# Kernel tuning notes

Hardware: AMD Instinct MI355X
Metric: run time of the kernel (lower is better)

The kernel has to match this reference:

```python
import jax, jax.numpy as jnp
import numpy as np

SIREN_OMEGA_0 = 30.0
EPS = 1e-4


def setup_inputs() -> dict:
    key = jax.random.key(0)
    ks = jax.random.split(key, 10)
    B, N, M, IN, OUT = 2, 16384, 1024, 256, 256
    x = jax.random.normal(ks[0], (B, N, IN), dtype=jnp.float32)
    query_coords = jax.random.normal(ks[1], (B, N, 3), dtype=jnp.float32)
    atomic_coords = jax.random.normal(ks[2], (B, M, 3), dtype=jnp.float32)
    # SIREN init (not is_first): bound = sqrt(6/in)/omega_0
    bound = (6.0 / IN) ** 0.5 / SIREN_OMEGA_0
    W = jax.random.uniform(ks[3], (OUT, IN), jnp.float32, -bound, bound)
    b = jax.random.uniform(ks[4], (OUT,), jnp.float32, -bound, bound)
    # freq_net: Linear(3,16) -> Softplus -> Linear(16,1), default torch init
    b1l = 1.0 / np.sqrt(3.0)
    fw1 = jax.random.uniform(ks[5], (16, 3), jnp.float32, -b1l, b1l)
    fb1 = jax.random.uniform(ks[6], (16,), jnp.float32, -b1l, b1l)
    b2l = 1.0 / np.sqrt(16.0)
    fw2 = jax.random.uniform(ks[7], (1, 16), jnp.float32, -b2l, b2l)
    fb2 = jax.random.uniform(ks[8], (1,), jnp.float32, -b2l, b2l)
    return {"x": x, "query_coords": query_coords, "atomic_coords": atomic_coords,
            "W": W, "b": b, "fw1": fw1, "fb1": fb1, "fw2": fw2, "fb2": fb2}


def reference(x, query_coords, atomic_coords, W, b, fw1, fb1, fw2, fb2):
    omega_base = SIREN_OMEGA_0
    # pre_activation = x @ W^T + b : [B, N, OUT]
    pre = jnp.einsum('bni,oi->bno', x, W) + b
    # freq_net(query_coords): Linear -> softplus -> Linear, clamp [0,5], nan->0
    h = jax.nn.softplus(jnp.einsum('bnd,hd->bnh', query_coords, fw1) + fb1)
    local_scale = jnp.einsum('bnh,oh->bno', h, fw2) + fb2  # [B, N, 1]
    local_scale = jnp.nan_to_num(jnp.clip(local_scale, 0.0, 5.0), nan=0.0)
    # pairwise distance [B, N, M] via broadcasted diff, then min over atoms
    diff = query_coords[:, :, None, :] - atomic_coords[:, None, :, :]  # [B,N,M,3]
    dist = jnp.sqrt(jnp.maximum(jnp.sum(diff * diff, axis=-1), EPS))
    min_dist = jnp.min(dist, axis=-1, keepdims=True)  # [B, N, 1]
    omega = omega_base * (1.0 + local_scale * jnp.exp(-min_dist))
    return jnp.sin(omega * pre)
```

## Files before the change

### kernel.cpp

```cpp
#include <hip/hip_runtime.h>
#include <hip/hip_bf16.h>

#define NPTS    32768
#define K_DIM   256
#define O_DIM   256
#define M_ATOMS 1024

typedef __attribute__((ext_vector_type(8))) short short8;
typedef __attribute__((ext_vector_type(4))) float f32x4;

__device__ __forceinline__ void split1(float v, short* h, short* l) {
  unsigned short hu = __bfloat16_as_ushort(__float2bfloat16(v));
  *h = (short)hu;
  float r = v - __uint_as_float((unsigned)hu << 16);
  *l = (short)__bfloat16_as_ushort(__float2bfloat16(r));
}

__device__ __forceinline__ void cvt8(const f32x4 f0, const f32x4 f1,
                                     short8* h, short8* l) {
#pragma unroll
  for (int j = 0; j < 4; ++j) {
    short hh, ll;
    split1(f0[j], &hh, &ll);
    (*h)[j] = hh; (*l)[j] = ll;
    split1(f1[j], &hh, &ll);
    (*h)[j + 4] = hh; (*l)[j + 4] = ll;
  }
}

__device__ __forceinline__ void async16(void* l, const void* g) {
  __builtin_amdgcn_global_load_lds(
      (const __attribute__((address_space(1))) void*)g,
      (__attribute__((address_space(3))) void*)l, 16, 0, 0);
}

__global__ __launch_bounds__(256) void wprep_kernel(const float* __restrict__ W,
                                                    unsigned short* __restrict__ whF,
                                                    unsigned short* __restrict__ wlF) {
  int t = blockIdx.x * 256 + threadIdx.x;
  int lane = t & 63;
  int ct = (t >> 6) & 15;
  int kc = t >> 10;
  int col = ct * 16 + (lane & 15);
  int k0 = kc * 32 + (lane >> 4) * 8;
  const float* src = W + (size_t)col * K_DIM + k0;
  f32x4 f0 = *(const f32x4*)(src);
  f32x4 f1 = *(const f32x4*)(src + 4);
  short8 h, l;
  cvt8(f0, f1, &h, &l);
  *(short8*)(whF + (size_t)t * 8) = h;
  *(short8*)(wlF + (size_t)t * 8) = l;
}

__global__ __launch_bounds__(512, 4) void fused_kernel(
    const float* __restrict__ x, const float* __restrict__ qc,
    const float* __restrict__ atoms,
    const unsigned short* __restrict__ whF, const unsigned short* __restrict__ wlF,
    const float* __restrict__ bias,
    const float* __restrict__ fw1, const float* __restrict__ fb1,
    const float* __restrict__ fw2, const float* __restrict__ fb2,
    float* __restrict__ out) {
  __shared__ char lds[65536];
  const int lane = threadIdx.x & 63;
  const int w = threadIdx.x >> 6;
  const int lrow = lane & 15;
  const int lk = lane >> 4;
  const int pb = (int)(blockIdx.x >> 2) * 256;
  const int cq = blockIdx.x & 3;
  const int pbase = pb + w * 32;

  {
    const char* whB = (const char*)whF;
    const char* wlB = (const char*)wlF;
    const int t = threadIdx.x;
    const int inner = (t & 255) * 16;
    const int kco = t >> 8;
#pragma unroll
    for (int p = 0; p < 4; ++p) {
      const int kc = p * 2 + kco;
      async16(lds + kc * 4096 + inner,
              whB + kc * 16384 + cq * 4096 + inner);
      async16(lds + 32768 + kc * 4096 + inner,
              wlB + kc * 16384 + cq * 4096 + inner);
    }
  }

  float bias_r[4];
#pragma unroll
  for (int ct = 0; ct < 4; ++ct) bias_r[ct] = bias[cq * 64 + ct * 16 + lrow];

  const float* xr0 = x + (size_t)(pbase + lrow) * K_DIM + lk * 8;
  const float* xr1 = xr0 + 16 * K_DIM;

  f32x4 c00 = *(const f32x4*)(xr0);
  f32x4 c01 = *(const f32x4*)(xr0 + 4);
  f32x4 c10 = *(const f32x4*)(xr1);
  f32x4 c11 = *(const f32x4*)(xr1 + 4);

  f32x4 acc[2][4];
#pragma unroll
  for (int t = 0; t < 2; ++t)
#pragma unroll
    for (int ct = 0; ct < 4; ++ct) acc[t][ct] = (f32x4){0.f, 0.f, 0.f, 0.f};

  __syncthreads();

#pragma unroll 1
  for (int kc = 0; kc < 8; ++kc) {
    f32x4 n00, n01, n10, n11;
    if (kc < 7) {
      const float* p0 = xr0 + (kc + 1) * 32;
      const float* p1 = xr1 + (kc + 1) * 32;
      n00 = *(const f32x4*)(p0); n01 = *(const f32x4*)(p0 + 4);
      n10 = *(const f32x4*)(p1); n11 = *(const f32x4*)(p1 + 4);
    }
    short8 ahi0, alo0, ahi1, alo1;
    cvt8(c00, c01, &ahi0, &alo0);
    cvt8(c10, c11, &ahi1, &alo1);
    const char* bp = lds + kc * 4096;
#pragma unroll
    for (int ct = 0; ct < 4; ++ct) {
      short8 bh = *(const short8*)(bp + ct * 1024 + lane * 16);
      short8 bl = *(const short8*)(bp + 32768 + ct * 1024 + lane * 16);
      acc[0][ct] = __builtin_amdgcn_mfma_f32_16x16x32_bf16(ahi0, bh, acc[0][ct], 0, 0, 0);
      acc[1][ct] = __builtin_amdgcn_mfma_f32_16x16x32_bf16(ahi1, bh, acc[1][ct], 0, 0, 0);
      acc[0][ct] = __builtin_amdgcn_mfma_f32_16x16x32_bf16(alo0, bh, acc[0][ct], 0, 0, 0);
      acc[1][ct] = __builtin_amdgcn_mfma_f32_16x16x32_bf16(alo1, bh, acc[1][ct], 0, 0, 0);
      acc[0][ct] = __builtin_amdgcn_mfma_f32_16x16x32_bf16(ahi0, bl, acc[0][ct], 0, 0, 0);
      acc[1][ct] = __builtin_amdgcn_mfma_f32_16x16x32_bf16(ahi1, bl, acc[1][ct], 0, 0, 0);
    }
    c00 = n00; c01 = n01; c10 = n10; c11 = n11;
  }

  __syncthreads();
  const int batch = pb >> 14;
  const float* A = atoms + (size_t)batch * M_ATOMS * 3;
  f32x4* at4 = (f32x4*)lds;
  {
    int i = threadIdx.x * 2;
    const float* ap = A + i * 3;
    float ax = ap[0], ay = ap[1], az = ap[2];
    at4[i] = (f32x4){ax, ay, az, ax * ax + ay * ay + az * az};
    ax = ap[3]; ay = ap[4]; az = ap[5];
    at4[i + 1] = (f32x4){ax, ay, az, ax * ax + ay * ay + az * az};
  }
  __syncthreads();

  const int pt = pbase + (lane & 31);
  const float qx = qc[(size_t)pt * 3 + 0];
  const float qy = qc[(size_t)pt * 3 + 1];
  const float qz = qc[(size_t)pt * 3 + 2];
  float m0 = 3.0e38f, m1 = 3.0e38f, m2 = 3.0e38f, m3 = 3.0e38f;
  const int i0 = (lane >> 5) * 512;
  for (int i = i0; i < i0 + 512; i += 4) {
    f32x4 v0 = at4[i + 0], v1 = at4[i + 1], v2 = at4[i + 2], v3 = at4[i + 3];
    float d;
    d = v0[0] * qx; d = __fmaf_rn(v0[1], qy, d); d = __fmaf_rn(v0[2], qz, d);
    m0 = fminf(m0, __fmaf_rn(d, -2.0f, v0[3]));
    d = v1[0] * qx; d = __fmaf_rn(v1[1], qy, d); d = __fmaf_rn(v1[2], qz, d);
    m1 = fminf(m1, __fmaf_rn(d, -2.0f, v1[3]));
    d = v2[0] * qx; d = __fmaf_rn(v2[1], qy, d); d = __fmaf_rn(v2[2], qz, d);
    m2 = fminf(m2, __fmaf_rn(d, -2.0f, v2[3]));
    d = v3[0] * qx; d = __fmaf_rn(v3[1], qy, d); d = __fmaf_rn(v3[2], qz, d);
    m3 = fminf(m3, __fmaf_rn(d, -2.0f, v3[3]));
  }
  float md = fminf(fminf(m0, m1), fminf(m2, m3));
  md = fminf(md, __shfl_xor(md, 32));
  md += qx * qx + qy * qy + qz * qz;
  float mind = sqrtf(fmaxf(md, 1.0e-4f));

  float facc = fb2[0];
#pragma unroll
  for (int j = 0; j < 16; ++j) {
    float z = fw1[j * 3 + 0] * qx + fw1[j * 3 + 1] * qy + fw1[j * 3 + 2] * qz + fb1[j];
    facc += fw2[j] * log1pf(__expf(z));
  }
  float ls = fminf(fmaxf(facc, 0.0f), 5.0f);
  float omega_l = 30.0f * (1.0f + ls * __expf(-mind));

  float om[2][4];
#pragma unroll
  for (int t = 0; t < 2; ++t)
#pragma unroll
    for (int j = 0; j < 4; ++j)
      om[t][j] = __shfl(omega_l, t * 16 + lk * 4 + j);

#pragma unroll
  for (int t = 0; t < 2; ++t) {
#pragma unroll
    for (int ct = 0; ct < 4; ++ct) {
#pragma unroll
      for (int j = 0; j < 4; ++j) {
        float pre = acc[t][ct][j] + bias_r[ct];
        out[(size_t)(pbase + t * 16 + lk * 4 + j) * O_DIM + cq * 64 + ct * 16 + lrow] =
            __sinf(om[t][j] * pre);
      }
    }
  }
}

extern "C" void kernel_launch(void* const* d_in, const int* in_sizes, int n_in,
                              void* d_out, int out_size, void* d_ws, size_t ws_size,
                              hipStream_t stream) {
  (void)in_sizes; (void)n_in; (void)out_size; (void)ws_size;
  const float* x     = (const float*)d_in[0];
  const float* qc    = (const float*)d_in[1];
  const float* atoms = (const float*)d_in[2];
  const float* W     = (const float*)d_in[3];
  const float* b     = (const float*)d_in[4];
  const float* fw1   = (const float*)d_in[5];
  const float* fb1   = (const float*)d_in[6];
  const float* fw2   = (const float*)d_in[7];
  const float* fb2   = (const float*)d_in[8];
  float* out = (float*)d_out;

  unsigned short* whF = (unsigned short*)d_ws;
  unsigned short* wlF = whF + 65536;

  wprep_kernel<<<32, 256, 0, stream>>>(W, whF, wlF);
  fused_kernel<<<512, 512, 0, stream>>>(x, qc, atoms, whF, wlF, b,
                                        fw1, fb1, fw2, fb2, out);
}
```

Measured before the change: 136.1 us.

## Restructure fused kernel into small 2-wave blocks with streamed per-k weight chunks

Each block now has 128 threads, and the grid grows to 2048 blocks, each covering 32 points by 128 output columns. Weight chunks are streamed into a small LDS buffer once per k-step instead of preloading the full 64KB. The distance minimum is split across both waves and combined through an LDS reduction. Block indices are swizzled, atom loads are vectorized, and softplus uses a stable max+log form. The aim is higher occupancy and less per-block LDS; the cost is more synchronisation per k-step and a redundant atom-distance scan per block.

```diff
diff --git a/kernel.cpp b/kernel.cpp
--- a/kernel.cpp
+++ b/kernel.cpp
@@ -52,7 +52,7 @@
   *(short8*)(wlF + (size_t)t * 8) = l;
 }
 
-__global__ __launch_bounds__(512, 4) void fused_kernel(
+__global__ __launch_bounds__(128, 4) void fused_kernel(
     const float* __restrict__ x, const float* __restrict__ qc,
     const float* __restrict__ atoms,
     const unsigned short* __restrict__ whF, const unsigned short* __restrict__ wlF,
@@ -60,99 +60,138 @@
     const float* __restrict__ fw1, const float* __restrict__ fb1,
     const float* __restrict__ fw2, const float* __restrict__ fb2,
     float* __restrict__ out) {
-  __shared__ char lds[65536];
+  __shared__ char lds[16640];
   const int lane = threadIdx.x & 63;
   const int w = threadIdx.x >> 6;
   const int lrow = lane & 15;
   const int lk = lane >> 4;
-  const int pb = (int)(blockIdx.x >> 2) * 256;
-  const int cq = blockIdx.x & 3;
-  const int pbase = pb + w * 32;
-
-  {
-    const char* whB = (const char*)whF;
-    const char* wlB = (const char*)wlF;
-    const int t = threadIdx.x;
-    const int inner = (t & 255) * 16;
-    const int kco = t >> 8;
-#pragma unroll
-    for (int p = 0; p < 4; ++p) {
-      const int kc = p * 2 + kco;
-      async16(lds + kc * 4096 + inner,
-              whB + kc * 16384 + cq * 4096 + inner);
-      async16(lds + 32768 + kc * 4096 + inner,
-              wlB + kc * 16384 + cq * 4096 + inner);
-    }
-  }
-
-  float bias_r[4];
-#pragma unroll
-  for (int ct = 0; ct < 4; ++ct) bias_r[ct] = bias[cq * 64 + ct * 16 + lrow];
+
+  const int p = blockIdx.x;
+  const int l = (p >> 3) + (p & 7) * 256;
+  const int u = l >> 1;
+  const int ch = l & 1;
+  const int pbase = u * 32;
+
+  const char* whB = (const char*)whF + ch * 8192;
+  const char* wlB = (const char*)wlF + ch * 8192;
+
+#pragma unroll
+  for (int r = 0; r < 4; ++r) {
+    async16(lds + r * 2048 + w * 1024,
+            whB + r * 2048 + w * 1024 + lane * 16);
+    async16(lds + 8192 + r * 2048 + w * 1024,
+            wlB + r * 2048 + w * 1024 + lane * 16);
+  }
 
   const float* xr0 = x + (size_t)(pbase + lrow) * K_DIM + lk * 8;
   const float* xr1 = xr0 + 16 * K_DIM;
 
-  f32x4 c00 = *(const f32x4*)(xr0);
-  f32x4 c01 = *(const f32x4*)(xr0 + 4);
-  f32x4 c10 = *(const f32x4*)(xr1);
-  f32x4 c11 = *(const f32x4*)(xr1 + 4);
-
-  f32x4 acc[2][4];
+  f32x4 c00 = *(const f32x4*)(xr0), c01 = *(const f32x4*)(xr0 + 4);
+  f32x4 c10 = *(const f32x4*)(xr1), c11 = *(const f32x4*)(xr1 + 4);
+
+  f32x4 acc[2][8];
 #pragma unroll
   for (int t = 0; t < 2; ++t)
 #pragma unroll
-    for (int ct = 0; ct < 4; ++ct) acc[t][ct] = (f32x4){0.f, 0.f, 0.f, 0.f};
-
-  __syncthreads();
+    for (int ct = 0; ct < 8; ++ct) acc[t][ct] = (f32x4){0.f, 0.f, 0.f, 0.f};
 
 #pragma unroll 1
   for (int kc = 0; kc < 8; ++kc) {
-    f32x4 n00, n01, n10, n11;
+    short8 ahi0, alo0, ahi1, alo1;
+    cvt8(c00, c01, &ahi0, &alo0);
+    cvt8(c10, c11, &ahi1, &alo1);
+    __syncthreads();
+
     if (kc < 7) {
       const float* p0 = xr0 + (kc + 1) * 32;
       const float* p1 = xr1 + (kc + 1) * 32;
-      n00 = *(const f32x4*)(p0); n01 = *(const f32x4*)(p0 + 4);
-      n10 = *(const f32x4*)(p1); n11 = *(const f32x4*)(p1 + 4);
-    }
-    short8 ahi0, alo0, ahi1, alo1;
-    cvt8(c00, c01, &ahi0, &alo0);
-    cvt8(c10, c11, &ahi1, &alo1);
-    const char* bp = lds + kc * 4096;
-#pragma unroll
-    for (int ct = 0; ct < 4; ++ct) {
-      short8 bh = *(const short8*)(bp + ct * 1024 + lane * 16);
-      short8 bl = *(const short8*)(bp + 32768 + ct * 1024 + lane * 16);
-      acc[0][ct] = __builtin_amdgcn_mfma_f32_16x16x32_bf16(ahi0, bh, acc[0][ct], 0, 0, 0);
-      acc[1][ct] = __builtin_amdgcn_mfma_f32_16x16x32_bf16(ahi1, bh, acc[1][ct], 0, 0, 0);
-      acc[0][ct] = __builtin_amdgcn_mfma_f32_16x16x32_bf16(alo0, bh, acc[0][ct], 0, 0, 0);
-      acc[1][ct] = __builtin_amdgcn_mfma_f32_16x16x32_bf16(alo1, bh, acc[1][ct], 0, 0, 0);
-      acc[0][ct] = __builtin_amdgcn_mfma_f32_16x16x32_bf16(ahi0, bl, acc[0][ct], 0, 0, 0);
-      acc[1][ct] = __builtin_amdgcn_mfma_f32_16x16x32_bf16(ahi1, bl, acc[1][ct], 0, 0, 0);
-    }
-    c00 = n00; c01 = n01; c10 = n10; c11 = n11;
-  }
-
-  __syncthreads();
-  const int batch = pb >> 14;
+      c00 = *(const f32x4*)(p0); c01 = *(const f32x4*)(p0 + 4);
+      c10 = *(const f32x4*)(p1); c11 = *(const f32x4*)(p1 + 4);
+    }
+
+#pragma unroll
+    for (int g = 0; g < 2; ++g) {
+      const char* bp = lds + g * 4096 + lane * 16;
+      short8 b0 = *(const short8*)(bp);
+      short8 b1 = *(const short8*)(bp + 1024);
+      short8 b2 = *(const short8*)(bp + 2048);
+      short8 b3 = *(const short8*)(bp + 3072);
+      const int c0 = g * 4;
+      acc[0][c0+0] = __builtin_amdgcn_mfma_f32_16x16x32_bf16(ahi0, b0, acc[0][c0+0], 0, 0, 0);
+      acc[0][c0+1] = __builtin_amdgcn_mfma_f32_16x16x32_bf16(ahi0, b1, acc[0][c0+1], 0, 0, 0);
+      acc[0][c0+2] = __builtin_amdgcn_mfma_f32_16x16x32_bf16(ahi0, b2, acc[0][c0+2], 0, 0, 0);
+      acc[0][c0+3] = __builtin_amdgcn_mfma_f32_16x16x32_bf16(ahi0, b3, acc[0][c0+3], 0, 0, 0);
+      acc[1][c0+0] = __builtin_amdgcn_mfma_f32_16x16x32_bf16(ahi1, b0, acc[1][c0+0], 0, 0, 0);
+      acc[1][c0+1] = __builtin_amdgcn_mfma_f32_16x16x32_bf16(ahi1, b1, acc[1][c0+1], 0, 0, 0);
+      acc[1][c0+2] = __builtin_amdgcn_mfma_f32_16x16x32_bf16(ahi1, b2, acc[1][c0+2], 0, 0, 0);
+      acc[1][c0+3] = __builtin_amdgcn_mfma_f32_16x16x32_bf16(ahi1, b3, acc[1][c0+3], 0, 0, 0);
+      acc[0][c0+0] = __builtin_amdgcn_mfma_f32_16x16x32_bf16(alo0, b0, acc[0][c0+0], 0, 0, 0);
+      acc[0][c0+1] = __builtin_amdgcn_mfma_f32_16x16x32_bf16(alo0, b1, acc[0][c0+1], 0, 0, 0);
+      acc[0][c0+2] = __builtin_amdgcn_mfma_f32_16x16x32_bf16(alo0, b2, acc[0][c0+2], 0, 0, 0);
+      acc[0][c0+3] = __builtin_amdgcn_mfma_f32_16x16x32_bf16(alo0, b3, acc[0][c0+3], 0, 0, 0);
+      acc[1][c0+0] = __builtin_amdgcn_mfma_f32_16x16x32_bf16(alo1, b0, acc[1][c0+0], 0, 0, 0);
+      acc[1][c0+1] = __builtin_amdgcn_mfma_f32_16x16x32_bf16(alo1, b1, acc[1][c0+1], 0, 0, 0);
+      acc[1][c0+2] = __builtin_amdgcn_mfma_f32_16x16x32_bf16(alo1, b2, acc[1][c0+2], 0, 0, 0);
+      acc[1][c0+3] = __builtin_amdgcn_mfma_f32_16x16x32_bf16(alo1, b3, acc[1][c0+3], 0, 0, 0);
+    }
+#pragma unroll
+    for (int g = 0; g < 2; ++g) {
+      const char* bp = lds + 8192 + g * 4096 + lane * 16;
+      short8 b0 = *(const short8*)(bp);
+      short8 b1 = *(const short8*)(bp + 1024);
+      short8 b2 = *(const short8*)(bp + 2048);
+      short8 b3 = *(const short8*)(bp + 3072);
+      const int c0 = g * 4;
+      acc[0][c0+0] = __builtin_amdgcn_mfma_f32_16x16x32_bf16(ahi0, b0, acc[0][c0+0], 0, 0, 0);
+      acc[0][c0+1] = __builtin_amdgcn_mfma_f32_16x16x32_bf16(ahi0, b1, acc[0][c0+1], 0, 0, 0);
+      acc[0][c0+2] = __builtin_amdgcn_mfma_f32_16x16x32_bf16(ahi0, b2, acc[0][c0+2], 0, 0, 0);
+      acc[0][c0+3] = __builtin_amdgcn_mfma_f32_16x16x32_bf16(ahi0, b3, acc[0][c0+3], 0, 0, 0);
+      acc[1][c0+0] = __builtin_amdgcn_mfma_f32_16x16x32_bf16(ahi1, b0, acc[1][c0+0], 0, 0, 0);
+      acc[1][c0+1] = __builtin_amdgcn_mfma_f32_16x16x32_bf16(ahi1, b1, acc[1][c0+1], 0, 0, 0);
+      acc[1][c0+2] = __builtin_amdgcn_mfma_f32_16x16x32_bf16(ahi1, b2, acc[1][c0+2], 0, 0, 0);
+      acc[1][c0+3] = __builtin_amdgcn_mfma_f32_16x16x32_bf16(ahi1, b3, acc[1][c0+3], 0, 0, 0);
+    }
+    __syncthreads();
+    if (kc < 7) {
+      const char* gh = whB + (kc + 1) * 16384;
+      const char* gl = wlB + (kc + 1) * 16384;
+#pragma unroll
+      for (int r = 0; r < 4; ++r) {
+        async16(lds + r * 2048 + w * 1024,
+                gh + r * 2048 + w * 1024 + lane * 16);
+        async16(lds + 8192 + r * 2048 + w * 1024,
+                gl + r * 2048 + w * 1024 + lane * 16);
+      }
+    }
+  }
+
+  const int batch = pbase >> 14;
   const float* A = atoms + (size_t)batch * M_ATOMS * 3;
   f32x4* at4 = (f32x4*)lds;
   {
-    int i = threadIdx.x * 2;
-    const float* ap = A + i * 3;
-    float ax = ap[0], ay = ap[1], az = ap[2];
-    at4[i] = (f32x4){ax, ay, az, ax * ax + ay * ay + az * az};
-    ax = ap[3]; ay = ap[4]; az = ap[5];
-    at4[i + 1] = (f32x4){ax, ay, az, ax * ax + ay * ay + az * az};
+    const int t = threadIdx.x;
+    const f32x4* ap = (const f32x4*)(A + t * 24);
+    f32x4 a0 = ap[0], a1 = ap[1], a2 = ap[2], a3 = ap[3], a4 = ap[4], a5 = ap[5];
+    f32x4* d = at4 + t * 8;
+    d[0] = (f32x4){a0[0], a0[1], a0[2], a0[0]*a0[0] + a0[1]*a0[1] + a0[2]*a0[2]};
+    d[1] = (f32x4){a0[3], a1[0], a1[1], a0[3]*a0[3] + a1[0]*a1[0] + a1[1]*a1[1]};
+    d[2] = (f32x4){a1[2], a1[3], a2[0], a1[2]*a1[2] + a1[3]*a1[3] + a2[0]*a2[0]};
+    d[3] = (f32x4){a2[1], a2[2], a2[3], a2[1]*a2[1] + a2[2]*a2[2] + a2[3]*a2[3]};
+    d[4] = (f32x4){a3[0], a3[1], a3[2], a3[0]*a3[0] + a3[1]*a3[1] + a3[2]*a3[2]};
+    d[5] = (f32x4){a3[3], a4[0], a4[1], a3[3]*a3[3] + a4[0]*a4[0] + a4[1]*a4[1]};
+    d[6] = (f32x4){a4[2], a4[3], a5[0], a4[2]*a4[2] + a4[3]*a4[3] + a5[0]*a5[0]};
+    d[7] = (f32x4){a5[1], a5[2], a5[3], a5[1]*a5[1] + a5[2]*a5[2] + a5[3]*a5[3]};
   }
   __syncthreads();
 
-  const int pt = pbase + (lane & 31);
+  const int pp = lane & 31;
+  const int pt = pbase + pp;
   const float qx = qc[(size_t)pt * 3 + 0];
   const float qy = qc[(size_t)pt * 3 + 1];
   const float qz = qc[(size_t)pt * 3 + 2];
   float m0 = 3.0e38f, m1 = 3.0e38f, m2 = 3.0e38f, m3 = 3.0e38f;
-  const int i0 = (lane >> 5) * 512;
-  for (int i = i0; i < i0 + 512; i += 4) {
+  const int i0 = w * 512 + (lane >> 5) * 256;
+  for (int i = i0; i < i0 + 256; i += 4) {
     f32x4 v0 = at4[i + 0], v1 = at4[i + 1], v2 = at4[i + 2], v3 = at4[i + 3];
     float d;
     d = v0[0] * qx; d = __fmaf_rn(v0[1], qy, d); d = __fmaf_rn(v0[2], qz, d);
@@ -166,6 +205,10 @@
   }
   float md = fminf(fminf(m0, m1), fminf(m2, m3));
   md = fminf(md, __shfl_xor(md, 32));
+  float* red = (float*)(lds + 16384);
+  if (lane < 32) red[w * 32 + lane] = md;
+  __syncthreads();
+  md = fminf(md, red[(w ^ 1) * 32 + pp]);
   md += qx * qx + qy * qy + qz * qz;
   float mind = sqrtf(fmaxf(md, 1.0e-4f));
 
@@ -173,7 +216,7 @@
 #pragma unroll
   for (int j = 0; j < 16; ++j) {
     float z = fw1[j * 3 + 0] * qx + fw1[j * 3 + 1] * qy + fw1[j * 3 + 2] * qz + fb1[j];
-    facc += fw2[j] * log1pf(__expf(z));
+    facc += fw2[j] * (fmaxf(z, 0.0f) + __logf(1.0f + __expf(-fabsf(z))));
   }
   float ls = fminf(fmaxf(facc, 0.0f), 5.0f);
   float omega_l = 30.0f * (1.0f + ls * __expf(-mind));
@@ -186,13 +229,14 @@
       om[t][j] = __shfl(omega_l, t * 16 + lk * 4 + j);
 
 #pragma unroll
-  for (int t = 0; t < 2; ++t) {
-#pragma unroll
-    for (int ct = 0; ct < 4; ++ct) {
+  for (int ct = 0; ct < 8; ++ct) {
+    float bv = bias[ch * 128 + ct * 16 + lrow];
+#pragma unroll
+    for (int t = 0; t < 2; ++t) {
 #pragma unroll
       for (int j = 0; j < 4; ++j) {
-        float pre = acc[t][ct][j] + bias_r[ct];
-        out[(size_t)(pbase + t * 16 + lk * 4 + j) * O_DIM + cq * 64 + ct * 16 + lrow] =
+        float pre = acc[t][ct][j] + bv;
+        out[(size_t)(pbase + t * 16 + lk * 4 + j) * O_DIM + ch * 128 + ct * 16 + lrow] =
             __sinf(om[t][j] * pre);
       }
     }
@@ -218,6 +262,6 @@
   unsigned short* wlF = whF + 65536;
 
   wprep_kernel<<<32, 256, 0, stream>>>(W, whF, wlF);
-  fused_kernel<<<512, 512, 0, stream>>>(x, qc, atoms, whF, wlF, b,
-                                        fw1, fb1, fw2, fb2, out);
-}
+  fused_kernel<<<2048, 128, 0, stream>>>(x, qc, atoms, whF, wlF, b,
+                                         fw1, fb1, fw2, fb2, out);
+}
```

Result: slower. 139.6 us (+2.6%).

## Restructure fused kernel to 64-point blocks covering all output columns

Applied to the files above, without the earlier changes.

Each block now handles 64 points and all 256 output columns with 4 waves, each wave owning 64 columns and a 4x4 MFMA tile. The old scheme tiled points by column quarter, so x was re-read per quarter and the atom min-distance was recomputed 4 times per point; the new one does the distance scan once per point, split across waves and reduced through LDS. Weights now stream from global/L2 into registers with double buffering instead of being staged in LDS. The trade is more registers per thread and a lower occupancy bound, plus a softplus rewritten in a numerically stable form.

```diff
diff --git a/kernel.cpp b/kernel.cpp
--- a/kernel.cpp
+++ b/kernel.cpp
@@ -26,12 +26,6 @@
     split1(f1[j], &hh, &ll);
     (*h)[j + 4] = hh; (*l)[j + 4] = ll;
   }
-}
-
-__device__ __forceinline__ void async16(void* l, const void* g) {
-  __builtin_amdgcn_global_load_lds(
-      (const __attribute__((address_space(1))) void*)g,
-      (__attribute__((address_space(3))) void*)l, 16, 0, 0);
 }
 
 __global__ __launch_bounds__(256) void wprep_kernel(const float* __restrict__ W,
@@ -52,7 +46,7 @@
   *(short8*)(wlF + (size_t)t * 8) = l;
 }
 
-__global__ __launch_bounds__(512, 4) void fused_kernel(
+__global__ __launch_bounds__(256, 2) void fused_kernel(
     const float* __restrict__ x, const float* __restrict__ qc,
     const float* __restrict__ atoms,
     const unsigned short* __restrict__ whF, const unsigned short* __restrict__ wlF,
@@ -60,140 +54,140 @@
     const float* __restrict__ fw1, const float* __restrict__ fb1,
     const float* __restrict__ fw2, const float* __restrict__ fb2,
     float* __restrict__ out) {
-  __shared__ char lds[65536];
-  const int lane = threadIdx.x & 63;
-  const int w = threadIdx.x >> 6;
+  __shared__ f32x4 at4[M_ATOMS];
+  __shared__ float red[4][64];
+  __shared__ float omg[64];
+
+  const int tid = threadIdx.x;
+  const int lane = tid & 63;
+  const int w = tid >> 6;
   const int lrow = lane & 15;
   const int lk = lane >> 4;
-  const int pb = (int)(blockIdx.x >> 2) * 256;
-  const int cq = blockIdx.x & 3;
-  const int pbase = pb + w * 32;
-
-  {
-    const char* whB = (const char*)whF;
-    const char* wlB = (const char*)wlF;
-    const int t = threadIdx.x;
-    const int inner = (t & 255) * 16;
-    const int kco = t >> 8;
-#pragma unroll
-    for (int p = 0; p < 4; ++p) {
-      const int kc = p * 2 + kco;
-      async16(lds + kc * 4096 + inner,
-              whB + kc * 16384 + cq * 4096 + inner);
-      async16(lds + 32768 + kc * 4096 + inner,
-              wlB + kc * 16384 + cq * 4096 + inner);
-    }
-  }
-
-  float bias_r[4];
-#pragma unroll
-  for (int ct = 0; ct < 4; ++ct) bias_r[ct] = bias[cq * 64 + ct * 16 + lrow];
-
-  const float* xr0 = x + (size_t)(pbase + lrow) * K_DIM + lk * 8;
-  const float* xr1 = xr0 + 16 * K_DIM;
-
-  f32x4 c00 = *(const f32x4*)(xr0);
-  f32x4 c01 = *(const f32x4*)(xr0 + 4);
-  f32x4 c10 = *(const f32x4*)(xr1);
-  f32x4 c11 = *(const f32x4*)(xr1 + 4);
-
-  f32x4 acc[2][4];
-#pragma unroll
-  for (int t = 0; t < 2; ++t)
-#pragma unroll
-    for (int ct = 0; ct < 4; ++ct) acc[t][ct] = (f32x4){0.f, 0.f, 0.f, 0.f};
-
-  __syncthreads();
-
-#pragma unroll 1
-  for (int kc = 0; kc < 8; ++kc) {
-    f32x4 n00, n01, n10, n11;
-    if (kc < 7) {
-      const float* p0 = xr0 + (kc + 1) * 32;
-      const float* p1 = xr1 + (kc + 1) * 32;
-      n00 = *(const f32x4*)(p0); n01 = *(const f32x4*)(p0 + 4);
-      n10 = *(const f32x4*)(p1); n11 = *(const f32x4*)(p1 + 4);
-    }
-    short8 ahi0, alo0, ahi1, alo1;
-    cvt8(c00, c01, &ahi0, &alo0);
-    cvt8(c10, c11, &ahi1, &alo1);
-    const char* bp = lds + kc * 4096;
-#pragma unroll
-    for (int ct = 0; ct < 4; ++ct) {
-      short8 bh = *(const short8*)(bp + ct * 1024 + lane * 16);
-      short8 bl = *(const short8*)(bp + 32768 + ct * 1024 + lane * 16);
-      acc[0][ct] = __builtin_amdgcn_mfma_f32_16x16x32_bf16(ahi0, bh, acc[0][ct], 0, 0, 0);
-      acc[1][ct] = __builtin_amdgcn_mfma_f32_16x16x32_bf16(ahi1, bh, acc[1][ct], 0, 0, 0);
-      acc[0][ct] = __builtin_amdgcn_mfma_f32_16x16x32_bf16(alo0, bh, acc[0][ct], 0, 0, 0);
-      acc[1][ct] = __builtin_amdgcn_mfma_f32_16x16x32_bf16(alo1, bh, acc[1][ct], 0, 0, 0);
-      acc[0][ct] = __builtin_amdgcn_mfma_f32_16x16x32_bf16(ahi0, bl, acc[0][ct], 0, 0, 0);
-      acc[1][ct] = __builtin_amdgcn_mfma_f32_16x16x32_bf16(ahi1, bl, acc[1][ct], 0, 0, 0);
-    }
-    c00 = n00; c01 = n01; c10 = n10; c11 = n11;
-  }
-
-  __syncthreads();
-  const int batch = pb >> 14;
+  const int pbase = blockIdx.x * 64;
+
+  const short8* BH = (const short8*)whF + (size_t)(w * 4) * 64 + lane;
+  const short8* BL = (const short8*)wlF + (size_t)(w * 4) * 64 + lane;
+  short8 bh[4], bl[4], nh[4], nl[4];
+#pragma unroll
+  for (int ct = 0; ct < 4; ++ct) {
+    bh[ct] = BH[ct * 64];
+    bl[ct] = BL[ct * 64];
+  }
+  const float* xr = x + (size_t)(pbase + lrow) * K_DIM + lk * 8;
+  f32x4 r0[4], r1[4];
+#pragma unroll
+  for (int t = 0; t < 4; ++t) {
+    r0[t] = *(const f32x4*)(xr + t * 16 * K_DIM);
+    r1[t] = *(const f32x4*)(xr + t * 16 * K_DIM + 4);
+  }
+
+  const int batch = pbase >> 14;
   const float* A = atoms + (size_t)batch * M_ATOMS * 3;
-  f32x4* at4 = (f32x4*)lds;
-  {
-    int i = threadIdx.x * 2;
-    const float* ap = A + i * 3;
+#pragma unroll
+  for (int j = 0; j < 4; ++j) {
+    int i = tid + j * 256;
+    const float* ap = A + (size_t)i * 3;
     float ax = ap[0], ay = ap[1], az = ap[2];
     at4[i] = (f32x4){ax, ay, az, ax * ax + ay * ay + az * az};
-    ax = ap[3]; ay = ap[4]; az = ap[5];
-    at4[i + 1] = (f32x4){ax, ay, az, ax * ax + ay * ay + az * az};
   }
   __syncthreads();
 
-  const int pt = pbase + (lane & 31);
+  const int pt = pbase + lane;
   const float qx = qc[(size_t)pt * 3 + 0];
   const float qy = qc[(size_t)pt * 3 + 1];
   const float qz = qc[(size_t)pt * 3 + 2];
-  float m0 = 3.0e38f, m1 = 3.0e38f, m2 = 3.0e38f, m3 = 3.0e38f;
-  const int i0 = (lane >> 5) * 512;
-  for (int i = i0; i < i0 + 512; i += 4) {
-    f32x4 v0 = at4[i + 0], v1 = at4[i + 1], v2 = at4[i + 2], v3 = at4[i + 3];
-    float d;
-    d = v0[0] * qx; d = __fmaf_rn(v0[1], qy, d); d = __fmaf_rn(v0[2], qz, d);
-    m0 = fminf(m0, __fmaf_rn(d, -2.0f, v0[3]));
-    d = v1[0] * qx; d = __fmaf_rn(v1[1], qy, d); d = __fmaf_rn(v1[2], qz, d);
-    m1 = fminf(m1, __fmaf_rn(d, -2.0f, v1[3]));
-    d = v2[0] * qx; d = __fmaf_rn(v2[1], qy, d); d = __fmaf_rn(v2[2], qz, d);
-    m2 = fminf(m2, __fmaf_rn(d, -2.0f, v2[3]));
-    d = v3[0] * qx; d = __fmaf_rn(v3[1], qy, d); d = __fmaf_rn(v3[2], qz, d);
-    m3 = fminf(m3, __fmaf_rn(d, -2.0f, v3[3]));
-  }
-  float md = fminf(fminf(m0, m1), fminf(m2, m3));
-  md = fminf(md, __shfl_xor(md, 32));
-  md += qx * qx + qy * qy + qz * qz;
-  float mind = sqrtf(fmaxf(md, 1.0e-4f));
-
-  float facc = fb2[0];
-#pragma unroll
-  for (int j = 0; j < 16; ++j) {
-    float z = fw1[j * 3 + 0] * qx + fw1[j * 3 + 1] * qy + fw1[j * 3 + 2] * qz + fb1[j];
-    facc += fw2[j] * log1pf(__expf(z));
-  }
-  float ls = fminf(fmaxf(facc, 0.0f), 5.0f);
-  float omega_l = 30.0f * (1.0f + ls * __expf(-mind));
-
-  float om[2][4];
-#pragma unroll
-  for (int t = 0; t < 2; ++t)
-#pragma unroll
-    for (int j = 0; j < 4; ++j)
-      om[t][j] = __shfl(omega_l, t * 16 + lk * 4 + j);
-
-#pragma unroll
-  for (int t = 0; t < 2; ++t) {
-#pragma unroll
-    for (int ct = 0; ct < 4; ++ct) {
+  {
+    float m0 = 3.0e38f, m1 = 3.0e38f, m2 = 3.0e38f, m3 = 3.0e38f;
+    const int i0 = w * 256;
+    for (int i = i0; i < i0 + 256; i += 4) {
+      f32x4 v0 = at4[i + 0], v1 = at4[i + 1], v2 = at4[i + 2], v3 = at4[i + 3];
+      float d;
+      d = v0[0] * qx; d = __fmaf_rn(v0[1], qy, d); d = __fmaf_rn(v0[2], qz, d);
+      m0 = fminf(m0, __fmaf_rn(d, -2.0f, v0[3]));
+      d = v1[0] * qx; d = __fmaf_rn(v1[1], qy, d); d = __fmaf_rn(v1[2], qz, d);
+      m1 = fminf(m1, __fmaf_rn(d, -2.0f, v1[3]));
+      d = v2[0] * qx; d = __fmaf_rn(v2[1], qy, d); d = __fmaf_rn(v2[2], qz, d);
+      m2 = fminf(m2, __fmaf_rn(d, -2.0f, v2[3]));
+      d = v3[0] * qx; d = __fmaf_rn(v3[1], qy, d); d = __fmaf_rn(v3[2], qz, d);
+      m3 = fminf(m3, __fmaf_rn(d, -2.0f, v3[3]));
+    }
+    red[w][lane] = fminf(fminf(m0, m1), fminf(m2, m3));
+  }
+  __syncthreads();
+  if (w == 0) {
+    float md = fminf(fminf(red[0][lane], red[1][lane]),
+                     fminf(red[2][lane], red[3][lane]));
+    md += qx * qx + qy * qy + qz * qz;
+    float mind = sqrtf(fmaxf(md, 1.0e-4f));
+    float facc = fb2[0];
+#pragma unroll
+    for (int j = 0; j < 16; ++j) {
+      float z = fw1[j * 3 + 0] * qx + fw1[j * 3 + 1] * qy + fw1[j * 3 + 2] * qz + fb1[j];
+      facc += fw2[j] * (fmaxf(z, 0.0f) + __logf(1.0f + __expf(-fabsf(z))));
+    }
+    float ls = fminf(fmaxf(facc, 0.0f), 5.0f);
+    omg[lane] = 30.0f * (1.0f + ls * __expf(-mind));
+  }
+  __syncthreads();
+
+  short8 ahi[4], alo[4];
+#pragma unroll
+  for (int t = 0; t < 4; ++t) cvt8(r0[t], r1[t], &ahi[t], &alo[t]);
+
+  f32x4 acc[4][4];
+#pragma unroll
+  for (int t = 0; t < 4; ++t)
+#pragma unroll
+    for (int ct = 0; ct < 4; ++ct) acc[t][ct] = (f32x4){0.f, 0.f, 0.f, 0.f};
+
+#pragma unroll 2
+  for (int kc = 0; kc < 8; ++kc) {
+    if (kc < 7) {
+#pragma unroll
+      for (int ct = 0; ct < 4; ++ct) {
+        nh[ct] = BH[(kc + 1) * 1024 + ct * 64];
+        nl[ct] = BL[(kc + 1) * 1024 + ct * 64];
+      }
+#pragma unroll
+      for (int t = 0; t < 4; ++t) {
+        r0[t] = *(const f32x4*)(xr + t * 16 * K_DIM + (kc + 1) * 32);
+        r1[t] = *(const f32x4*)(xr + t * 16 * K_DIM + (kc + 1) * 32 + 4);
+      }
+    }
+#pragma unroll
+    for (int ct = 0; ct < 4; ++ct)
+#pragma unroll
+      for (int t = 0; t < 4; ++t)
+        acc[t][ct] = __builtin_amdgcn_mfma_f32_16x16x32_bf16(ahi[t], bh[ct], acc[t][ct], 0, 0, 0);
+#pragma unroll
+    for (int ct = 0; ct < 4; ++ct)
+#pragma unroll
+      for (int t = 0; t < 4; ++t)
+        acc[t][ct] = __builtin_amdgcn_mfma_f32_16x16x32_bf16(alo[t], bh[ct], acc[t][ct], 0, 0, 0);
+#pragma unroll
+    for (int ct = 0; ct < 4; ++ct)
+#pragma unroll
+      for (int t = 0; t < 4; ++t)
+        acc[t][ct] = __builtin_amdgcn_mfma_f32_16x16x32_bf16(ahi[t], bl[ct], acc[t][ct], 0, 0, 0);
+    if (kc < 7) {
+#pragma unroll
+      for (int t = 0; t < 4; ++t) cvt8(r0[t], r1[t], &ahi[t], &alo[t]);
+#pragma unroll
+      for (int ct = 0; ct < 4; ++ct) { bh[ct] = nh[ct]; bl[ct] = nl[ct]; }
+    }
+  }
+
+#pragma unroll
+  for (int ct = 0; ct < 4; ++ct) {
+    float bv = bias[w * 64 + ct * 16 + lrow];
+#pragma unroll
+    for (int t = 0; t < 4; ++t) {
 #pragma unroll
       for (int j = 0; j < 4; ++j) {
-        float pre = acc[t][ct][j] + bias_r[ct];
-        out[(size_t)(pbase + t * 16 + lk * 4 + j) * O_DIM + cq * 64 + ct * 16 + lrow] =
-            __sinf(om[t][j] * pre);
+        float om = omg[t * 16 + lk * 4 + j];
+        float pre = acc[t][ct][j] + bv;
+        out[(size_t)(pbase + t * 16 + lk * 4 + j) * O_DIM + w * 64 + ct * 16 + lrow] =
+            __sinf(om * pre);
       }
     }
   }
@@ -218,6 +212,6 @@
   unsigned short* wlF = whF + 65536;
 
   wprep_kernel<<<32, 256, 0, stream>>>(W, whF, wlF);
-  fused_kernel<<<512, 512, 0, stream>>>(x, qc, atoms, whF, wlF, b,
+  fused_kernel<<<512, 256, 0, stream>>>(x, qc, atoms, whF, wlF, b,
                                         fw1, fb1, fw2, fb2, out);
 }
```

New measurement: 121.3 us. 1.12x faster.
